# Kernel tuning notes

Measured on AMD Instinct MI355X. Metric: run time of the kernel, lower is better.

The kernel has to match this reference:

```python
import jax, jax.numpy as jnp
import numpy as np


def setup_inputs() -> dict:
    key = jax.random.key(0)
    ks = jax.random.split(key, 4)
    C, CK = 256, 32  # in_channels, in_channels // 8
    B, H, W = 16, 64, 64
    x = jax.random.normal(ks[0], (B, C, H, W), dtype=jnp.float32)
    # conv1x1 weights (kernel spatial dims squeezed), scaled like kaiming-ish init
    Wq = jax.random.normal(ks[1], (CK, C), dtype=jnp.float32) / np.sqrt(C)
    Wk = jax.random.normal(ks[2], (CK, C), dtype=jnp.float32) / np.sqrt(C)
    Wv = jax.random.normal(ks[3], (C, C), dtype=jnp.float32) / np.sqrt(C)
    bq = jnp.zeros((CK,), jnp.float32)
    bk = jnp.zeros((CK,), jnp.float32)
    bv = jnp.zeros((C,), jnp.float32)
    alpha = jnp.zeros((1,), jnp.float32)  # nn.Parameter(torch.zeros(1))
    return {"x": x, "Wq": Wq, "bq": bq, "Wk": Wk, "bk": bk,
            "Wv": Wv, "bv": bv, "alpha": alpha}


def reference(x, Wq, bq, Wk, bk, Wv, bv, alpha):
    B, C, H, W = x.shape
    N = H * W
    xf = x.reshape(B, C, N)  # [B, C, N]
    # 1x1 convs == per-pixel linear projections
    q = jnp.einsum('oc,bcn->bno', Wq, xf) + bq          # [B, N, CK]  (query, permuted)
    k = jnp.einsum('oc,bcn->bon', Wk, xf) + bk[:, None]  # [B, CK, N]
    v = jnp.einsum('oc,bcn->bon', Wv, xf) + bv[:, None]  # [B, C, N]
    # NOTE: faithful to source -- no 1/sqrt(d) scaling
    scores = jnp.einsum('bno,bom->bnm', q, k)            # [B, N, N]
    attn = jax.nn.softmax(scores, axis=-1)               # softmax over keys
    # out = value @ attention^T : out[:, :, i] = sum_j attn[i, j] * v[:, :, j]
    out = jnp.einsum('bcm,bnm->bcn', v, attn).reshape(B, C, H, W)
    return alpha[0] * out + x
```

## Files before the change

kernel.cpp:

```cpp
#include <hip/hip_runtime.h>
#include <cstdint>
#include <cstddef>

#define BN 16
#define CC 256
#define CKD 32
#define NN 4096

typedef __attribute__((ext_vector_type(8))) short s8v;
typedef __attribute__((ext_vector_type(4))) float f4v;
typedef __attribute__((ext_vector_type(4))) unsigned int u4v;
typedef __attribute__((ext_vector_type(2))) unsigned int u2v;
typedef unsigned short ushort_t;

#define L2E 1.44269504088896340736f

__device__ __forceinline__ ushort_t f2bf(float f) {
    union { float f; uint32_t u; } v; v.f = f;
    uint32_t u = v.u + 0x7FFFu + ((v.u >> 16) & 1u);
    return (ushort_t)(u >> 16);
}
__device__ __forceinline__ uint32_t fbits(float f) {
    union { float f; uint32_t u; } v; v.f = f; return v.u;
}
__device__ __forceinline__ float exp2_hw(float x) {
    float r; asm("v_exp_f32 %0, %1" : "=v"(r) : "v"(x)); return r;
}
__device__ __forceinline__ uint32_t pkbf(float lo, float hi) {
    return __builtin_amdgcn_perm(fbits(hi), fbits(lo), 0x07060302u);
}

__global__ __launch_bounds__(256) void proj_all(
    const float* __restrict__ x,
    const float* __restrict__ Wq, const float* __restrict__ bq,
    const float* __restrict__ Wk, const float* __restrict__ bk,
    const float* __restrict__ Wv, const float* __restrict__ bv,
    ushort_t* __restrict__ qw, ushort_t* __restrict__ kw, ushort_t* __restrict__ vw)
{
    __shared__ __align__(16) ushort_t As[64 * 264];

    int b  = blockIdx.z;
    int m0 = blockIdx.y * 64;
    int n0 = blockIdx.x * 128;
    int tid = threadIdx.x;
    int wave = tid >> 6, lane = tid & 63;
    int lq = lane & 15, quad = lane >> 4;

    {
        int arow = tid >> 2;
        int kseg = (tid & 3) * 64;
        int am = m0 + arow;
        const float* wrow;
        if (am < 32)       wrow = Wq + (size_t)am * CC;
        else if (am < 64)  wrow = Wk + (size_t)(am - 32) * CC;
        else               wrow = Wv + (size_t)(am - 64) * CC;
#pragma unroll
        for (int g = 0; g < 8; g++) {
            f4v f0 = *reinterpret_cast<const f4v*>(wrow + kseg + g * 8);
            f4v f1 = *reinterpret_cast<const f4v*>(wrow + kseg + g * 8 + 4);
            s8v p;
            p[0] = (short)f2bf(f0[0]); p[1] = (short)f2bf(f0[1]);
            p[2] = (short)f2bf(f0[2]); p[3] = (short)f2bf(f0[3]);
            p[4] = (short)f2bf(f1[0]); p[5] = (short)f2bf(f1[1]);
            p[6] = (short)f2bf(f1[2]); p[7] = (short)f2bf(f1[3]);
            *reinterpret_cast<s8v*>(&As[arow * 264 + kseg + g * 8]) = p;
        }
    }
    __syncthreads();

    f4v acc[4][2];
#pragma unroll
    for (int i = 0; i < 4; i++)
#pragma unroll
        for (int j = 0; j < 2; j++) acc[i][j] = (f4v){0.f, 0.f, 0.f, 0.f};

    const float* xb = x + (size_t)b * CC * NN + n0 + wave * 32 + lq;

#pragma unroll 2
    for (int h = 0; h < 8; h++) {
        s8v bb[2];
#pragma unroll
        for (int nt = 0; nt < 2; nt++) {
            const float* src = xb + (size_t)(h * 32 + quad * 8) * NN + nt * 16;
            float t0 = src[0 * NN];
            float t1 = src[1 * NN];
            float t2 = src[2 * NN];
            float t3 = src[3 * NN];
            float t4 = src[4 * NN];
            float t5 = src[5 * NN];
            float t6 = src[6 * NN];
            float t7 = src[7 * NN];
            s8v p;
            p[0] = (short)f2bf(t0); p[1] = (short)f2bf(t1);
            p[2] = (short)f2bf(t2); p[3] = (short)f2bf(t3);
            p[4] = (short)f2bf(t4); p[5] = (short)f2bf(t5);
            p[6] = (short)f2bf(t6); p[7] = (short)f2bf(t7);
            bb[nt] = p;
        }
        s8v a[4];
#pragma unroll
        for (int mt = 0; mt < 4; mt++)
            a[mt] = *reinterpret_cast<const s8v*>(
                &As[(mt * 16 + lq) * 264 + h * 32 + quad * 8]);
#pragma unroll
        for (int mt = 0; mt < 4; mt++)
#pragma unroll
            for (int nt = 0; nt < 2; nt++)
                acc[mt][nt] = __builtin_amdgcn_mfma_f32_16x16x32_bf16(
                    a[mt], bb[nt], acc[mt][nt], 0, 0, 0);
    }

#pragma unroll
    for (int mt = 0; mt < 4; mt++) {
#pragma unroll
        for (int r = 0; r < 4; r++) {
            int mm = m0 + mt * 16 + quad * 4 + r;
            float bias = (mm < 32) ? bq[mm] : (mm < 64 ? bk[mm - 32] : bv[mm - 64]);
#pragma unroll
            for (int nt = 0; nt < 2; nt++) {
                int n = n0 + wave * 32 + nt * 16 + lq;
                float val = acc[mt][nt][r] + bias;
                if (mm < 32) val *= L2E;
                ushort_t obf = f2bf(val);
                if (mm < 32)
                    qw[((size_t)b * NN + n) * CKD + mm] = obf;
                else if (mm < 64)
                    kw[((size_t)b * NN + n) * CKD + (mm - 32)] = obf;
                else
                    vw[((size_t)b * CC + (mm - 64)) * NN + n] = obf;
            }
        }
    }
}

__global__ __launch_bounds__(512, 4) void attn(
    const ushort_t* __restrict__ qw, const ushort_t* __restrict__ kw,
    const ushort_t* __restrict__ vw, const float* __restrict__ x,
    const float* __restrict__ alpha, float* __restrict__ out)
{
    __shared__ __align__(16) ushort_t Pl[2][128 * 72];
    __shared__ __align__(16) ushort_t Kl[2][64 * 32];
    __shared__ float lL[128];

    int b = blockIdx.y;
    int q0 = blockIdx.x * 128;
    int tid = threadIdx.x;
    int wq = tid >> 6, lane = tid & 63;
    int lq = lane & 15, quad = lane >> 4;

    const ushort_t* kbase = kw + (size_t)b * NN * CKD;
    const ushort_t* vbase = vw + (size_t)b * CC * NN;

    int krow = tid >> 3;
    int kcol = (tid & 7) * 4;
    const ushort_t* ksrc = kbase + (size_t)krow * CKD + kcol;

    int kro[4];
#pragma unroll
    for (int nt = 0; nt < 4; nt++)
        kro[nt] = (32 * (nt >> 1) + 2 * (lq & 12) + 4 * (nt & 1) + (lq & 3)) * 32 + quad * 8;

    const ushort_t* vrow0 = vbase + (size_t)(wq * 32 + lq) * NN;
    const ushort_t* vrow1 = vbase + (size_t)(wq * 32 + 16 + lq) * NN;

    const s8v qf = *reinterpret_cast<const s8v*>(
        qw + ((size_t)b * NN + q0 + wq * 16 + lq) * CKD + quad * 8);

    f4v acc[8][2];
#pragma unroll
    for (int i = 0; i < 8; i++) {
        acc[i][0] = (f4v){0.f, 0.f, 0.f, 0.f};
        acc[i][1] = (f4v){0.f, 0.f, 0.f, 0.f};
    }
    float srow = 0.f;

    u2v k0 = *reinterpret_cast<const u2v*>(ksrc);
    u2v k1 = *reinterpret_cast<const u2v*>(ksrc + (size_t)64 * CKD);
    u2v kst = *reinterpret_cast<const u2v*>(ksrc + (size_t)128 * CKD);
    s8v v00 = *reinterpret_cast<const s8v*>(vrow0 + quad * 8);
    s8v v01 = *reinterpret_cast<const s8v*>(vrow0 + 32 + quad * 8);
    s8v v10 = *reinterpret_cast<const s8v*>(vrow1 + quad * 8);
    s8v v11 = *reinterpret_cast<const s8v*>(vrow1 + 32 + quad * 8);
    *reinterpret_cast<u2v*>(&Kl[0][krow * 32 + kcol]) = k0;
    *reinterpret_cast<u2v*>(&Kl[1][krow * 32 + kcol]) = k1;
    __syncthreads();

    for (int kt = 0; kt < 64; kt++) {
        const int cur = kt & 1;

        s8v pa0, pa1;
        {
            s8v kf0 = *reinterpret_cast<const s8v*>(&Kl[cur][kro[0]]);
            s8v kf1 = *reinterpret_cast<const s8v*>(&Kl[cur][kro[1]]);
            f4v sA = __builtin_amdgcn_mfma_f32_16x16x32_bf16(kf0, qf, (f4v){0.f,0.f,0.f,0.f}, 0, 0, 0);
            f4v sB = __builtin_amdgcn_mfma_f32_16x16x32_bf16(kf1, qf, (f4v){0.f,0.f,0.f,0.f}, 0, 0, 0);
            s8v kf2 = *reinterpret_cast<const s8v*>(&Kl[cur][kro[2]]);
            s8v kf3 = *reinterpret_cast<const s8v*>(&Kl[cur][kro[3]]);
            f4v sC = __builtin_amdgcn_mfma_f32_16x16x32_bf16(kf2, qf, (f4v){0.f,0.f,0.f,0.f}, 0, 0, 0);
            f4v sD = __builtin_amdgcn_mfma_f32_16x16x32_bf16(kf3, qf, (f4v){0.f,0.f,0.f,0.f}, 0, 0, 0);
            float a0 = exp2_hw(sA[0]), a1 = exp2_hw(sA[1]), a2 = exp2_hw(sA[2]), a3 = exp2_hw(sA[3]);
            float b0 = exp2_hw(sB[0]), b1 = exp2_hw(sB[1]), b2 = exp2_hw(sB[2]), b3 = exp2_hw(sB[3]);
            srow += ((a0 + a1) + (a2 + a3)) + ((b0 + b1) + (b2 + b3));
            union { u4v u; s8v s; } t0;
            t0.u[0] = pkbf(a0, a1); t0.u[1] = pkbf(a2, a3);
            t0.u[2] = pkbf(b0, b1); t0.u[3] = pkbf(b2, b3);
            pa0 = t0.s;
            float c0 = exp2_hw(sC[0]), c1 = exp2_hw(sC[1]), c2 = exp2_hw(sC[2]), c3 = exp2_hw(sC[3]);
            float d0 = exp2_hw(sD[0]), d1 = exp2_hw(sD[1]), d2 = exp2_hw(sD[2]), d3 = exp2_hw(sD[3]);
            srow += ((c0 + c1) + (c2 + c3)) + ((d0 + d1) + (d2 + d3));
            union { u4v u; s8v s; } t1;
            t1.u[0] = pkbf(c0, c1); t1.u[1] = pkbf(c2, c3);
            t1.u[2] = pkbf(d0, d1); t1.u[3] = pkbf(d2, d3);
            pa1 = t1.s;
        }

        {
            int prow = (wq * 16 + lq) * 72;
            *reinterpret_cast<s8v*>(&Pl[cur][prow + quad * 8]) = pa0;
            *reinterpret_cast<s8v*>(&Pl[cur][prow + 32 + quad * 8]) = pa1;
        }

        __syncthreads();
        __builtin_amdgcn_sched_barrier(0);

        *reinterpret_cast<u2v*>(&Kl[cur][krow * 32 + kcol]) = kst;

        __builtin_amdgcn_s_setprio(1);
#pragma unroll
        for (int qt = 0; qt < 8; qt++) {
            s8v pA0 = *reinterpret_cast<const s8v*>(&Pl[cur][(qt * 16 + lq) * 72 + quad * 8]);
            s8v pA1 = *reinterpret_cast<const s8v*>(&Pl[cur][(qt * 16 + lq) * 72 + 32 + quad * 8]);
            acc[qt][0] = __builtin_amdgcn_mfma_f32_16x16x32_bf16(pA0, v00, acc[qt][0], 0, 0, 0);
            acc[qt][0] = __builtin_amdgcn_mfma_f32_16x16x32_bf16(pA1, v01, acc[qt][0], 0, 0, 0);
            acc[qt][1] = __builtin_amdgcn_mfma_f32_16x16x32_bf16(pA0, v10, acc[qt][1], 0, 0, 0);
            acc[qt][1] = __builtin_amdgcn_mfma_f32_16x16x32_bf16(pA1, v11, acc[qt][1], 0, 0, 0);
        }
        __builtin_amdgcn_s_setprio(0);

        {
            int kbn = (kt + 1 < 64 ? kt + 1 : 63) * 64;
            v00 = *reinterpret_cast<const s8v*>(vrow0 + kbn + quad * 8);
            v01 = *reinterpret_cast<const s8v*>(vrow0 + kbn + 32 + quad * 8);
            v10 = *reinterpret_cast<const s8v*>(vrow1 + kbn + quad * 8);
            v11 = *reinterpret_cast<const s8v*>(vrow1 + kbn + 32 + quad * 8);
            int kn = (kt + 3 < 64 ? kt + 3 : 63) * 64;
            kst = *reinterpret_cast<const u2v*>(ksrc + (size_t)kn * CKD);
        }
    }

    srow += __shfl_xor(srow, 16, 64);
    srow += __shfl_xor(srow, 32, 64);
    if (quad == 0) lL[wq * 16 + lq] = srow;
    __syncthreads();

    float a0 = alpha[0];
#pragma unroll
    for (int qt = 0; qt < 8; qt++) {
        float li[4];
#pragma unroll
        for (int r = 0; r < 4; r++) li[r] = 1.0f / lL[qt * 16 + quad * 4 + r];
#pragma unroll
        for (int ct = 0; ct < 2; ct++) {
            int c = wq * 32 + ct * 16 + lq;
            size_t idx = ((size_t)b * CC + c) * NN + q0 + qt * 16 + quad * 4;
            f4v xv = *reinterpret_cast<const f4v*>(x + idx);
            f4v o;
#pragma unroll
            for (int r = 0; r < 4; r++) o[r] = a0 * (acc[qt][ct][r] * li[r]) + xv[r];
            *reinterpret_cast<f4v*>(out + idx) = o;
        }
    }
}

extern "C" void kernel_launch(void* const* d_in, const int* in_sizes, int n_in,
                              void* d_out, int out_size, void* d_ws, size_t ws_size,
                              hipStream_t stream) {
    (void)in_sizes; (void)n_in; (void)out_size; (void)ws_size;
    const float* x     = (const float*)d_in[0];
    const float* Wq    = (const float*)d_in[1];
    const float* bq    = (const float*)d_in[2];
    const float* Wk    = (const float*)d_in[3];
    const float* bk    = (const float*)d_in[4];
    const float* Wv    = (const float*)d_in[5];
    const float* bv    = (const float*)d_in[6];
    const float* alpha = (const float*)d_in[7];
    float* out = (float*)d_out;

    char* ws = (char*)d_ws;
    ushort_t* qw = (ushort_t*)ws;
    ushort_t* kw = (ushort_t*)(ws + (size_t)BN * NN * CKD * 2);
    ushort_t* vw = (ushort_t*)(ws + (size_t)2 * BN * NN * CKD * 2);

    proj_all<<<dim3(NN / 128, 5, BN), 256, 0, stream>>>(x, Wq, bq, Wk, bk, Wv, bv, qw, kw, vw);
    attn    <<<dim3(NN / 128, BN), 512, 0, stream>>>(qw, kw, vw, x, alpha, out);
}
```

Before: 326.4 us.

## Retile PV per wave as 64x64 block, pad K LDS, XCD-aware grid remap

The PV stage now gives each wave a 64-query by 64-channel output tile instead of 128 queries by 32 channels. This halves the P-fragment LDS reads per MFMA and holds more V fragments in registers. The K shared buffer row stride is padded from 32 to 36 to avoid LDS bank conflicts. Both kernels switch to 1D grids with XCD-aware index remapping, so blocks sharing a batch or x tile land on the same XCD for L2 reuse. The cost is more register pressure for the V fragments and the 16 accumulators, which may affect occupancy at 512 threads with 4 waves per SIMD.

New measurement: 527.2 us. 1.62x slower.

```diff
diff --git a/kernel.cpp b/kernel.cpp
--- a/kernel.cpp
+++ b/kernel.cpp
@@ -39,9 +39,16 @@
 {
     __shared__ __align__(16) ushort_t As[64 * 264];
 
-    int b  = blockIdx.z;
-    int m0 = blockIdx.y * 64;
-    int n0 = blockIdx.x * 128;
+    int l = blockIdx.x;
+    int xcd = l & 7;
+    int t = l >> 3;
+    int slot = t / 5;
+    int mten = t - slot * 5;
+    int p = slot * 8 + xcd;
+    int b  = p >> 5;
+    int m0 = mten * 64;
+    int n0 = (p & 31) * 128;
+
     int tid = threadIdx.x;
     int wave = tid >> 6, lane = tid & 63;
     int lq = lane & 15, quad = lane >> 4;
@@ -58,12 +65,12 @@
         for (int g = 0; g < 8; g++) {
             f4v f0 = *reinterpret_cast<const f4v*>(wrow + kseg + g * 8);
             f4v f1 = *reinterpret_cast<const f4v*>(wrow + kseg + g * 8 + 4);
-            s8v p;
-            p[0] = (short)f2bf(f0[0]); p[1] = (short)f2bf(f0[1]);
-            p[2] = (short)f2bf(f0[2]); p[3] = (short)f2bf(f0[3]);
-            p[4] = (short)f2bf(f1[0]); p[5] = (short)f2bf(f1[1]);
-            p[6] = (short)f2bf(f1[2]); p[7] = (short)f2bf(f1[3]);
-            *reinterpret_cast<s8v*>(&As[arow * 264 + kseg + g * 8]) = p;
+            s8v p2;
+            p2[0] = (short)f2bf(f0[0]); p2[1] = (short)f2bf(f0[1]);
+            p2[2] = (short)f2bf(f0[2]); p2[3] = (short)f2bf(f0[3]);
+            p2[4] = (short)f2bf(f1[0]); p2[5] = (short)f2bf(f1[1]);
+            p2[6] = (short)f2bf(f1[2]); p2[7] = (short)f2bf(f1[3]);
+            *reinterpret_cast<s8v*>(&As[arow * 264 + kseg + g * 8]) = p2;
         }
     }
     __syncthreads();
@@ -90,12 +97,12 @@
             float t5 = src[5 * NN];
             float t6 = src[6 * NN];
             float t7 = src[7 * NN];
-            s8v p;
-            p[0] = (short)f2bf(t0); p[1] = (short)f2bf(t1);
-            p[2] = (short)f2bf(t2); p[3] = (short)f2bf(t3);
-            p[4] = (short)f2bf(t4); p[5] = (short)f2bf(t5);
-            p[6] = (short)f2bf(t6); p[7] = (short)f2bf(t7);
-            bb[nt] = p;
+            s8v p2;
+            p2[0] = (short)f2bf(t0); p2[1] = (short)f2bf(t1);
+            p2[2] = (short)f2bf(t2); p2[3] = (short)f2bf(t3);
+            p2[4] = (short)f2bf(t4); p2[5] = (short)f2bf(t5);
+            p2[6] = (short)f2bf(t6); p2[7] = (short)f2bf(t7);
+            bb[nt] = p2;
         }
         s8v a[4];
 #pragma unroll
@@ -139,14 +146,18 @@
     const float* __restrict__ alpha, float* __restrict__ out)
 {
     __shared__ __align__(16) ushort_t Pl[2][128 * 72];
-    __shared__ __align__(16) ushort_t Kl[2][64 * 32];
+    __shared__ __align__(16) ushort_t Kl[2][64 * 36];
     __shared__ float lL[128];
 
-    int b = blockIdx.y;
-    int q0 = blockIdx.x * 128;
+    int l = blockIdx.x;
+    int b = (l & 7) | (((l >> 3) & 1) << 3);
+    int q0 = (l >> 4) * 128;
+
     int tid = threadIdx.x;
     int wq = tid >> 6, lane = tid & 63;
     int lq = lane & 15, quad = lane >> 4;
+    int i64 = (wq >> 2) * 64;
+    int j64 = (wq & 3) * 64;
 
     const ushort_t* kbase = kw + (size_t)b * NN * CKD;
     const ushort_t* vbase = vw + (size_t)b * CC * NN;
@@ -158,31 +169,34 @@
     int kro[4];
 #pragma unroll
     for (int nt = 0; nt < 4; nt++)
-        kro[nt] = (32 * (nt >> 1) + 2 * (lq & 12) + 4 * (nt & 1) + (lq & 3)) * 32 + quad * 8;
-
-    const ushort_t* vrow0 = vbase + (size_t)(wq * 32 + lq) * NN;
-    const ushort_t* vrow1 = vbase + (size_t)(wq * 32 + 16 + lq) * NN;
+        kro[nt] = (32 * (nt >> 1) + 2 * (lq & 12) + 4 * (nt & 1) + (lq & 3)) * 36 + quad * 8;
+
+    const ushort_t* vr[4];
+#pragma unroll
+    for (int ct = 0; ct < 4; ct++)
+        vr[ct] = vbase + (size_t)(j64 + ct * 16 + lq) * NN;
 
     const s8v qf = *reinterpret_cast<const s8v*>(
         qw + ((size_t)b * NN + q0 + wq * 16 + lq) * CKD + quad * 8);
 
-    f4v acc[8][2];
-#pragma unroll
-    for (int i = 0; i < 8; i++) {
-        acc[i][0] = (f4v){0.f, 0.f, 0.f, 0.f};
-        acc[i][1] = (f4v){0.f, 0.f, 0.f, 0.f};
-    }
+    f4v acc[4][4];
+#pragma unroll
+    for (int i = 0; i < 4; i++)
+#pragma unroll
+        for (int j = 0; j < 4; j++) acc[i][j] = (f4v){0.f, 0.f, 0.f, 0.f};
     float srow = 0.f;
 
     u2v k0 = *reinterpret_cast<const u2v*>(ksrc);
     u2v k1 = *reinterpret_cast<const u2v*>(ksrc + (size_t)64 * CKD);
     u2v kst = *reinterpret_cast<const u2v*>(ksrc + (size_t)128 * CKD);
-    s8v v00 = *reinterpret_cast<const s8v*>(vrow0 + quad * 8);
-    s8v v01 = *reinterpret_cast<const s8v*>(vrow0 + 32 + quad * 8);
-    s8v v10 = *reinterpret_cast<const s8v*>(vrow1 + quad * 8);
-    s8v v11 = *reinterpret_cast<const s8v*>(vrow1 + 32 + quad * 8);
-    *reinterpret_cast<u2v*>(&Kl[0][krow * 32 + kcol]) = k0;
-    *reinterpret_cast<u2v*>(&Kl[1][krow * 32 + kcol]) = k1;
+    s8v vv[4][2];
+#pragma unroll
+    for (int ct = 0; ct < 4; ct++) {
+        vv[ct][0] = *reinterpret_cast<const s8v*>(vr[ct] + quad * 8);
+        vv[ct][1] = *reinterpret_cast<const s8v*>(vr[ct] + 32 + quad * 8);
+    }
+    *reinterpret_cast<u2v*>(&Kl[0][krow * 36 + kcol]) = k0;
+    *reinterpret_cast<u2v*>(&Kl[1][krow * 36 + kcol]) = k1;
     __syncthreads();
 
     for (int kt = 0; kt < 64; kt++) {
@@ -223,26 +237,29 @@
         __syncthreads();
         __builtin_amdgcn_sched_barrier(0);
 
-        *reinterpret_cast<u2v*>(&Kl[cur][krow * 32 + kcol]) = kst;
+        *reinterpret_cast<u2v*>(&Kl[cur][krow * 36 + kcol]) = kst;
 
         __builtin_amdgcn_s_setprio(1);
 #pragma unroll
-        for (int qt = 0; qt < 8; qt++) {
-            s8v pA0 = *reinterpret_cast<const s8v*>(&Pl[cur][(qt * 16 + lq) * 72 + quad * 8]);
-            s8v pA1 = *reinterpret_cast<const s8v*>(&Pl[cur][(qt * 16 + lq) * 72 + 32 + quad * 8]);
-            acc[qt][0] = __builtin_amdgcn_mfma_f32_16x16x32_bf16(pA0, v00, acc[qt][0], 0, 0, 0);
-            acc[qt][0] = __builtin_amdgcn_mfma_f32_16x16x32_bf16(pA1, v01, acc[qt][0], 0, 0, 0);
-            acc[qt][1] = __builtin_amdgcn_mfma_f32_16x16x32_bf16(pA0, v10, acc[qt][1], 0, 0, 0);
-            acc[qt][1] = __builtin_amdgcn_mfma_f32_16x16x32_bf16(pA1, v11, acc[qt][1], 0, 0, 0);
+        for (int qt = 0; qt < 4; qt++) {
+            int pr = (i64 + qt * 16 + lq) * 72;
+            s8v pA0 = *reinterpret_cast<const s8v*>(&Pl[cur][pr + quad * 8]);
+            s8v pA1 = *reinterpret_cast<const s8v*>(&Pl[cur][pr + 32 + quad * 8]);
+#pragma unroll
+            for (int ct = 0; ct < 4; ct++) {
+                acc[qt][ct] = __builtin_amdgcn_mfma_f32_16x16x32_bf16(pA0, vv[ct][0], acc[qt][ct], 0, 0, 0);
+                acc[qt][ct] = __builtin_amdgcn_mfma_f32_16x16x32_bf16(pA1, vv[ct][1], acc[qt][ct], 0, 0, 0);
+            }
         }
         __builtin_amdgcn_s_setprio(0);
 
         {
             int kbn = (kt + 1 < 64 ? kt + 1 : 63) * 64;
-            v00 = *reinterpret_cast<const s8v*>(vrow0 + kbn + quad * 8);
-            v01 = *reinterpret_cast<const s8v*>(vrow0 + kbn + 32 + quad * 8);
-            v10 = *reinterpret_cast<const s8v*>(vrow1 + kbn + quad * 8);
-            v11 = *reinterpret_cast<const s8v*>(vrow1 + kbn + 32 + quad * 8);
+#pragma unroll
+            for (int ct = 0; ct < 4; ct++) {
+                vv[ct][0] = *reinterpret_cast<const s8v*>(vr[ct] + kbn + quad * 8);
+                vv[ct][1] = *reinterpret_cast<const s8v*>(vr[ct] + kbn + 32 + quad * 8);
+            }
             int kn = (kt + 3 < 64 ? kt + 3 : 63) * 64;
             kst = *reinterpret_cast<const u2v*>(ksrc + (size_t)kn * CKD);
         }
@@ -255,14 +272,14 @@
 
     float a0 = alpha[0];
 #pragma unroll
-    for (int qt = 0; qt < 8; qt++) {
+    for (int qt = 0; qt < 4; qt++) {
         float li[4];
 #pragma unroll
-        for (int r = 0; r < 4; r++) li[r] = 1.0f / lL[qt * 16 + quad * 4 + r];
-#pragma unroll
-        for (int ct = 0; ct < 2; ct++) {
-            int c = wq * 32 + ct * 16 + lq;
-            size_t idx = ((size_t)b * CC + c) * NN + q0 + qt * 16 + quad * 4;
+        for (int r = 0; r < 4; r++) li[r] = 1.0f / lL[i64 + qt * 16 + quad * 4 + r];
+#pragma unroll
+        for (int ct = 0; ct < 4; ct++) {
+            int c = j64 + ct * 16 + lq;
+            size_t idx = ((size_t)b * CC + c) * NN + q0 + i64 + qt * 16 + quad * 4;
             f4v xv = *reinterpret_cast<const f4v*>(x + idx);
             f4v o;
 #pragma unroll
@@ -291,6 +308,6 @@
     ushort_t* kw = (ushort_t*)(ws + (size_t)BN * NN * CKD * 2);
     ushort_t* vw = (ushort_t*)(ws + (size_t)2 * BN * NN * CKD * 2);
 
-    proj_all<<<dim3(NN / 128, 5, BN), 256, 0, stream>>>(x, Wq, bq, Wk, bk, Wv, bv, qw, kw, vw);
-    attn    <<<dim3(NN / 128, BN), 512, 0, stream>>>(qw, kw, vw, x, alpha, out);
-}
+    proj_all<<<dim3(2560), 256, 0, stream>>>(x, Wq, bq, Wk, bk, Wv, bv, qw, kw, vw);
+    attn    <<<dim3(512), 512, 0, stream>>>(qw, kw, vw, x, alpha, out);
+}
```

## Load x tile once per block and loop over all projection row tiles

Applied to the files above, without the earlier changes.

The projection kernel now has each block own a 64-pixel slice of one batch and load its full column of x (converted to bf16) into registers once. It then loops over the five 64-row weight tiles, restaging each into shared memory, so x is no longer re-read from global memory five times. Q and K results are packed into 8-byte vector stores instead of scalar stores. The trade-offs are fewer blocks (1024 instead of 2560), extra weight restaging and barriers inside each block, and more registers held per thread.

Measured after the change: 318.8 us. 2.3% less time.

```diff
diff --git a/kernel.cpp b/kernel.cpp
--- a/kernel.cpp
+++ b/kernel.cpp
@@ -28,6 +28,9 @@
 }
 __device__ __forceinline__ uint32_t pkbf(float lo, float hi) {
     return __builtin_amdgcn_perm(fbits(hi), fbits(lo), 0x07060302u);
+}
+__device__ __forceinline__ uint32_t pkbf_rne(float lo, float hi) {
+    return (uint32_t)f2bf(lo) | ((uint32_t)f2bf(hi) << 16);
 }
 
 __global__ __launch_bounds__(256) void proj_all(
@@ -39,96 +42,110 @@
 {
     __shared__ __align__(16) ushort_t As[64 * 264];
 
-    int b  = blockIdx.z;
-    int m0 = blockIdx.y * 64;
-    int n0 = blockIdx.x * 128;
+    int b  = blockIdx.y;
+    int n0 = blockIdx.x * 64;
     int tid = threadIdx.x;
     int wave = tid >> 6, lane = tid & 63;
     int lq = lane & 15, quad = lane >> 4;
-
-    {
-        int arow = tid >> 2;
-        int kseg = (tid & 3) * 64;
-        int am = m0 + arow;
-        const float* wrow;
-        if (am < 32)       wrow = Wq + (size_t)am * CC;
-        else if (am < 64)  wrow = Wk + (size_t)(am - 32) * CC;
-        else               wrow = Wv + (size_t)(am - 64) * CC;
-#pragma unroll
-        for (int g = 0; g < 8; g++) {
-            f4v f0 = *reinterpret_cast<const f4v*>(wrow + kseg + g * 8);
-            f4v f1 = *reinterpret_cast<const f4v*>(wrow + kseg + g * 8 + 4);
-            s8v p;
-            p[0] = (short)f2bf(f0[0]); p[1] = (short)f2bf(f0[1]);
-            p[2] = (short)f2bf(f0[2]); p[3] = (short)f2bf(f0[3]);
-            p[4] = (short)f2bf(f1[0]); p[5] = (short)f2bf(f1[1]);
-            p[6] = (short)f2bf(f1[2]); p[7] = (short)f2bf(f1[3]);
-            *reinterpret_cast<s8v*>(&As[arow * 264 + kseg + g * 8]) = p;
-        }
-    }
-    __syncthreads();
-
-    f4v acc[4][2];
-#pragma unroll
-    for (int i = 0; i < 4; i++)
-#pragma unroll
-        for (int j = 0; j < 2; j++) acc[i][j] = (f4v){0.f, 0.f, 0.f, 0.f};
-
-    const float* xb = x + (size_t)b * CC * NN + n0 + wave * 32 + lq;
-
-#pragma unroll 2
+    int n = n0 + wave * 16 + lq;
+
+    const float* xb = x + (size_t)b * CC * NN + n;
+    s8v bb[8];
+#pragma unroll
     for (int h = 0; h < 8; h++) {
-        s8v bb[2];
-#pragma unroll
-        for (int nt = 0; nt < 2; nt++) {
-            const float* src = xb + (size_t)(h * 32 + quad * 8) * NN + nt * 16;
-            float t0 = src[0 * NN];
-            float t1 = src[1 * NN];
-            float t2 = src[2 * NN];
-            float t3 = src[3 * NN];
-            float t4 = src[4 * NN];
-            float t5 = src[5 * NN];
-            float t6 = src[6 * NN];
-            float t7 = src[7 * NN];
-            s8v p;
-            p[0] = (short)f2bf(t0); p[1] = (short)f2bf(t1);
-            p[2] = (short)f2bf(t2); p[3] = (short)f2bf(t3);
-            p[4] = (short)f2bf(t4); p[5] = (short)f2bf(t5);
-            p[6] = (short)f2bf(t6); p[7] = (short)f2bf(t7);
-            bb[nt] = p;
-        }
-        s8v a[4];
-#pragma unroll
-        for (int mt = 0; mt < 4; mt++)
-            a[mt] = *reinterpret_cast<const s8v*>(
-                &As[(mt * 16 + lq) * 264 + h * 32 + quad * 8]);
-#pragma unroll
-        for (int mt = 0; mt < 4; mt++)
-#pragma unroll
-            for (int nt = 0; nt < 2; nt++)
-                acc[mt][nt] = __builtin_amdgcn_mfma_f32_16x16x32_bf16(
-                    a[mt], bb[nt], acc[mt][nt], 0, 0, 0);
-    }
-
-#pragma unroll
-    for (int mt = 0; mt < 4; mt++) {
-#pragma unroll
-        for (int r = 0; r < 4; r++) {
-            int mm = m0 + mt * 16 + quad * 4 + r;
-            float bias = (mm < 32) ? bq[mm] : (mm < 64 ? bk[mm - 32] : bv[mm - 64]);
-#pragma unroll
-            for (int nt = 0; nt < 2; nt++) {
-                int n = n0 + wave * 32 + nt * 16 + lq;
-                float val = acc[mt][nt][r] + bias;
-                if (mm < 32) val *= L2E;
-                ushort_t obf = f2bf(val);
-                if (mm < 32)
-                    qw[((size_t)b * NN + n) * CKD + mm] = obf;
-                else if (mm < 64)
-                    kw[((size_t)b * NN + n) * CKD + (mm - 32)] = obf;
-                else
-                    vw[((size_t)b * CC + (mm - 64)) * NN + n] = obf;
+        const float* src = xb + (size_t)(h * 32 + quad * 8) * NN;
+        float t0 = src[0 * NN];
+        float t1 = src[1 * NN];
+        float t2 = src[2 * NN];
+        float t3 = src[3 * NN];
+        float t4 = src[4 * NN];
+        float t5 = src[5 * NN];
+        float t6 = src[6 * NN];
+        float t7 = src[7 * NN];
+        s8v p;
+        p[0] = (short)f2bf(t0); p[1] = (short)f2bf(t1);
+        p[2] = (short)f2bf(t2); p[3] = (short)f2bf(t3);
+        p[4] = (short)f2bf(t4); p[5] = (short)f2bf(t5);
+        p[6] = (short)f2bf(t6); p[7] = (short)f2bf(t7);
+        bb[h] = p;
+    }
+
+    int arow = tid >> 2;
+    int kseg = (tid & 3) * 64;
+
+    for (int mten = 0; mten < 5; mten++) {
+        int m0 = mten * 64;
+        __syncthreads();
+
+        {
+            int am = m0 + arow;
+            const float* wrow;
+            if (am < 32)       wrow = Wq + (size_t)am * CC;
+            else if (am < 64)  wrow = Wk + (size_t)(am - 32) * CC;
+            else               wrow = Wv + (size_t)(am - 64) * CC;
+#pragma unroll
+            for (int g = 0; g < 8; g++) {
+                f4v f0 = *reinterpret_cast<const f4v*>(wrow + kseg + g * 8);
+                f4v f1 = *reinterpret_cast<const f4v*>(wrow + kseg + g * 8 + 4);
+                s8v p;
+                p[0] = (short)f2bf(f0[0]); p[1] = (short)f2bf(f0[1]);
+                p[2] = (short)f2bf(f0[2]); p[3] = (short)f2bf(f0[3]);
+                p[4] = (short)f2bf(f1[0]); p[5] = (short)f2bf(f1[1]);
+                p[6] = (short)f2bf(f1[2]); p[7] = (short)f2bf(f1[3]);
+                *reinterpret_cast<s8v*>(&As[arow * 264 + kseg + g * 8]) = p;
             }
+        }
+        __syncthreads();
+
+        f4v acc[4];
+#pragma unroll
+        for (int i = 0; i < 4; i++) acc[i] = (f4v){0.f, 0.f, 0.f, 0.f};
+#pragma unroll
+        for (int h = 0; h < 8; h++) {
+            s8v a[4];
+#pragma unroll
+            for (int mt = 0; mt < 4; mt++)
+                a[mt] = *reinterpret_cast<const s8v*>(
+                    &As[(mt * 16 + lq) * 264 + h * 32 + quad * 8]);
+#pragma unroll
+            for (int mt = 0; mt < 4; mt++)
+                acc[mt] = __builtin_amdgcn_mfma_f32_16x16x32_bf16(
+                    a[mt], bb[h], acc[mt], 0, 0, 0);
+        }
+
+        if (mten == 0) {
+#pragma unroll
+            for (int mt = 0; mt < 2; mt++) {
+                int ck = mt * 16 + quad * 4;
+                float v0 = (acc[mt][0] + bq[ck + 0]) * L2E;
+                float v1 = (acc[mt][1] + bq[ck + 1]) * L2E;
+                float v2 = (acc[mt][2] + bq[ck + 2]) * L2E;
+                float v3 = (acc[mt][3] + bq[ck + 3]) * L2E;
+                u2v w;
+                w[0] = pkbf_rne(v0, v1);
+                w[1] = pkbf_rne(v2, v3);
+                *reinterpret_cast<u2v*>(qw + ((size_t)b * NN + n) * CKD + ck) = w;
+            }
+#pragma unroll
+            for (int mt = 0; mt < 2; mt++) {
+                int ck = mt * 16 + quad * 4;
+                float v0 = acc[mt + 2][0] + bk[ck + 0];
+                float v1 = acc[mt + 2][1] + bk[ck + 1];
+                float v2 = acc[mt + 2][2] + bk[ck + 2];
+                float v3 = acc[mt + 2][3] + bk[ck + 3];
+                u2v w;
+                w[0] = pkbf_rne(v0, v1);
+                w[1] = pkbf_rne(v2, v3);
+                *reinterpret_cast<u2v*>(kw + ((size_t)b * NN + n) * CKD + ck) = w;
+            }
+        } else {
+#pragma unroll
+            for (int mt = 0; mt < 4; mt++)
+#pragma unroll
+                for (int r = 0; r < 4; r++) {
+                    int c = (m0 - 64) + mt * 16 + quad * 4 + r;
+                    vw[((size_t)b * CC + c) * NN + n] = f2bf(acc[mt][r] + bv[c]);
+                }
         }
     }
 }
@@ -291,6 +308,6 @@
     ushort_t* kw = (ushort_t*)(ws + (size_t)BN * NN * CKD * 2);
     ushort_t* vw = (ushort_t*)(ws + (size_t)2 * BN * NN * CKD * 2);
 
-    proj_all<<<dim3(NN / 128, 5, BN), 256, 0, stream>>>(x, Wq, bq, Wk, bk, Wv, bv, qw, kw, vw);
+    proj_all<<<dim3(64, BN), 256, 0, stream>>>(x, Wq, bq, Wk, bk, Wv, bv, qw, kw, vw);
     attn    <<<dim3(NN / 128, BN), 512, 0, stream>>>(qw, kw, vw, x, alpha, out);
 }
```
